# Kernel tuning notes

Hardware: AMD Instinct MI355X
Metric: run time of the kernel (lower is better)

The kernel has to match this reference:

```python
import jax, jax.numpy as jnp
import numpy as np

CODEBOOK_SIZE = 1024
LATENT_DIM = 64
BETA = 0.25

def setup_inputs() -> dict:
    key = jax.random.key(0)
    k1, k2 = jax.random.split(key)
    B, C, T = 32, LATENT_DIM, 4096
    x = jax.random.normal(k1, (B, C, T), dtype=jnp.float32)
    # codebook initialized uniform(-1/K, 1/K) as in the torch module
    emb = jax.random.uniform(k2, (CODEBOOK_SIZE, LATENT_DIM), dtype=jnp.float32,
                             minval=-1.0 / CODEBOOK_SIZE, maxval=1.0 / CODEBOOK_SIZE)
    return {"x": x, "emb": emb}

def reference(x, emb):
    B, C, T = x.shape  # C == LATENT_DIM
    xf = jnp.transpose(x, (0, 2, 1)).reshape(B * T, C)  # [BT, D]
    d = (jnp.sum(xf * xf, axis=-1, keepdims=True)
         + jnp.sum(emb * emb, axis=-1)[None, :]
         - 2.0 * jnp.matmul(xf, emb.T))  # [BT, K]
    idx = jnp.argmin(d, axis=-1)  # [BT] int
    q = emb[idx].reshape(B, T, C).transpose(0, 2, 1)  # [B, C, T]
    commitment_loss = BETA * jnp.mean((jax.lax.stop_gradient(q) - x) ** 2)
    codebook_loss = jnp.mean((q - jax.lax.stop_gradient(x)) ** 2)
    quant_out = x + jax.lax.stop_gradient(q - x)  # straight-through
    return quant_out, codebook_loss, commitment_loss, idx.reshape(B, T)
```

## Files before the change

### kernel.cpp

```cpp
#include <hip/hip_runtime.h>


typedef unsigned long long u64;
typedef unsigned short u16;
typedef __attribute__((ext_vector_type(8))) short bf8_t;
typedef __attribute__((ext_vector_type(4))) float f4_t;

#define KCB 1024
#define DD 64
#define BB 32
#define TT 4096
#define BT (BB * TT)
#define NELEM (BB * DD * TT)

#define RPB 128
#define NT 16
#define FB_MAX 48
#define BAND 4e-5f

#define WS_LOSS 0
#define WS_E2 64
#define WS_EH 2048
#define WS_EL 34816

static __device__ __forceinline__ u16 bf16rte(float f) {
    unsigned u = __float_as_uint(f);
    return (u16)((u + 0x7FFFu + ((u >> 16) & 1u)) >> 16);
}
static __device__ __forceinline__ unsigned flipf(float f) {
    unsigned u = __float_as_uint(f);
    return (u & 0x80000000u) ? ~u : (u | 0x80000000u);
}
static __device__ __forceinline__ int fragidx(int n, int d) {
    return 1024 * (n >> 4) + 512 * (d >> 5) + 128 * ((d >> 3) & 3)
         + 8 * (n & 15) + (d & 7);
}

__global__ void vq_prep(const float* __restrict__ emb, float* __restrict__ ws) {
#pragma clang fp contract(off)
    const int tid = threadIdx.x;
    const int kl = tid >> 6, d = tid & 63;
    const int k = blockIdx.x * 4 + kl;
    if (blockIdx.x == 0 && tid == 0) ws[WS_LOSS] = 0.0f;
    __shared__ float sq[4][64];
    __shared__ float rsh[4][8];
    float v = emb[(size_t)k * DD + d];
    u16 hb = bf16rte(v);
    float hv = __uint_as_float((unsigned)hb << 16);
    u16 lb = bf16rte(v - hv);
    u16* ehg = (u16*)(ws + WS_EH) + 4096 * (k >> 6);
    u16* elg = (u16*)(ws + WS_EL) + 4096 * (k >> 6);
    const int ia = fragidx(k & 63, d);
    ehg[ia] = hb; elg[ia] = lb;
    sq[kl][d] = v * v;
    __syncthreads();
    if (tid < 32) {
        const int g = tid >> 3, j = tid & 7;
        float r = sq[g][j];
#pragma unroll
        for (int i = 1; i < 8; ++i) r += sq[g][8 * i + j];
        rsh[g][j] = r;
    }
    __syncthreads();
    if (tid < 4) {
        const float* r = rsh[tid];
        ws[WS_E2 + blockIdx.x * 4 + tid] =
            ((r[0] + r[1]) + (r[2] + r[3])) + ((r[4] + r[5]) + (r[6] + r[7]));
    }
}

__launch_bounds__(256, 4)
__global__ void vq_main(const float* __restrict__ x, const float* __restrict__ emb,
                        float* __restrict__ out, float* __restrict__ ws) {
#pragma clang fp contract(off)
    const int tid = threadIdx.x;
    const int lane = tid & 63;
    const int w = __builtin_amdgcn_readfirstlane(tid >> 6);
    const int l15 = lane & 15, q = lane >> 4;

    const int row0 = blockIdx.x * RPB;
    const int b = row0 >> 12;
    const int t0 = row0 & (TT - 1);

    __shared__ __align__(16) char arena[32768];
    u16* xhT = (u16*)arena;
    u16* xlT = (u16*)(arena + 16384);
    float* efs = (float*)arena;
    float* xfb = (float*)(arena + 16640);

    __shared__ float e2l[KCB];
    __shared__ float Srow[RPB];
    __shared__ int kwin[RPB];
    __shared__ int fbrows[FB_MAX];
    __shared__ int fbcnt;
    __shared__ float bsum;

    if (tid == 0) { fbcnt = 0; bsum = 0.0f; }
#pragma unroll
    for (int i = tid; i < KCB; i += 256) e2l[i] = ws[WS_E2 + i];

    if (tid < RPB) {
        const int r = tid;
        const float* xr = x + (size_t)b * DD * TT + t0 + r;
        const int gb = 1024 * (r >> 4);
        float rr[8];
#pragma unroll
        for (int i = 0; i < 64; i += 8) {
#pragma unroll
            for (int j = 0; j < 8; ++j) {
                float v = xr[(size_t)(i + j) * TT];
                if (i == 0) rr[j] = v * v; else rr[j] += v * v;
                u16 hb = bf16rte(v);
                float hv = __uint_as_float((unsigned)hb << 16);
                u16 lb = bf16rte(v - hv);
                const int ia = gb + fragidx(r & 15, i + j);
                xhT[ia] = hb; xlT[ia] = lb;
            }
        }
        Srow[r] = ((rr[0] + rr[1]) + (rr[2] + rr[3])) + ((rr[4] + rr[5]) + (rr[6] + rr[7]));
    }
    __syncthreads();

    bf8_t ah[2][2], al[2][2];
#pragma unroll
    for (int g = 0; g < 2; ++g) {
        const int gg = 2 * w + g;
        ah[g][0] = *(const bf8_t*)&xhT[1024 * gg + 8 * lane];
        ah[g][1] = *(const bf8_t*)&xhT[1024 * gg + 512 + 8 * lane];
        al[g][0] = *(const bf8_t*)&xlT[1024 * gg + 8 * lane];
        al[g][1] = *(const bf8_t*)&xlT[1024 * gg + 512 + 8 * lane];
    }
    float Sv[8];
#pragma unroll
    for (int g = 0; g < 2; ++g)
#pragma unroll
        for (int rg = 0; rg < 4; ++rg)
            Sv[4 * g + rg] = Srow[32 * w + 16 * g + 4 * q + rg];

    float v1[8], v2[8], kf[8];
#pragma unroll
    for (int s = 0; s < 8; ++s) { v1[s] = 3.4e38f; v2[s] = 3.4e38f; kf[s] = 0.0f; }

    const u16* ehg = (const u16*)(ws + WS_EH);
    const u16* elg = (const u16*)(ws + WS_EL);

#pragma unroll 1
    for (int T = 0; T < NT; ++T) {
#pragma unroll
        for (int cg = 0; cg < 4; ++cg) {
            const int kb = 64 * T + 16 * cg;
            const u16* bhp = ehg + 4096 * T + 1024 * cg;
            const u16* blp = elg + 4096 * T + 1024 * cg;
            bf8_t bh0 = *(const bf8_t*)&bhp[8 * lane];
            bf8_t bh1 = *(const bf8_t*)&bhp[512 + 8 * lane];
            bf8_t bl0 = *(const bf8_t*)&blp[8 * lane];
            bf8_t bl1 = *(const bf8_t*)&blp[512 + 8 * lane];
            const float e2v = e2l[kb + l15];
            const float kcol = (float)(kb + l15);
#pragma unroll
            for (int g = 0; g < 2; ++g) {
                f4_t acc = (f4_t){0.f, 0.f, 0.f, 0.f};
                acc = __builtin_amdgcn_mfma_f32_16x16x32_bf16(ah[g][0], bh0, acc, 0, 0, 0);
                acc = __builtin_amdgcn_mfma_f32_16x16x32_bf16(ah[g][0], bl0, acc, 0, 0, 0);
                acc = __builtin_amdgcn_mfma_f32_16x16x32_bf16(al[g][0], bh0, acc, 0, 0, 0);
                acc = __builtin_amdgcn_mfma_f32_16x16x32_bf16(ah[g][1], bh1, acc, 0, 0, 0);
                acc = __builtin_amdgcn_mfma_f32_16x16x32_bf16(ah[g][1], bl1, acc, 0, 0, 0);
                acc = __builtin_amdgcn_mfma_f32_16x16x32_bf16(al[g][1], bh1, acc, 0, 0, 0);
#pragma unroll
                for (int rg = 0; rg < 4; ++rg) {
                    const int s = 4 * g + rg;
                    float ck = Sv[s] + e2v;
                    float u = __builtin_fmaf(-2.0f, acc[rg], ck);
                    bool lt = u < v1[s];
                    float sp = lt ? v1[s] : u;
                    v2[s] = fminf(v2[s], sp);
                    kf[s] = lt ? kcol : kf[s];
                    v1[s] = fminf(v1[s], u);
                }
            }
        }
    }

#pragma unroll
    for (int m = 1; m < 16; m <<= 1) {
#pragma unroll
        for (int s = 0; s < 8; ++s) {
            float ov1 = __shfl_xor(v1[s], m, 16);
            float okf = __shfl_xor(kf[s], m, 16);
            float ov2 = __shfl_xor(v2[s], m, 16);
            float nmx = fmaxf(v1[s], ov1);
            v2[s] = fminf(fminf(v2[s], ov2), nmx);
            bool lt = ov1 < v1[s];
            kf[s] = lt ? okf : kf[s];
            v1[s] = fminf(v1[s], ov1);
        }
    }
    if (l15 == 0) {
#pragma unroll
        for (int g = 0; g < 2; ++g)
#pragma unroll
            for (int rg = 0; rg < 4; ++rg) {
                const int s = 4 * g + rg;
                const int r = 32 * w + 16 * g + 4 * q + rg;
                kwin[r] = (int)kf[s];
                if (v2[s] <= v1[s] + BAND) {
                    int i = atomicAdd(&fbcnt, 1);
                    if (i < FB_MAX) fbrows[i] = r;
                }
            }
    }
    __syncthreads();

    const int cnt = min(fbcnt, FB_MAX);
    if (cnt > 0) {
        for (int i = tid; i < cnt * 64; i += 256) {
            int fi = i >> 6, l = i & 63;
            xfb[fi * 65 + l] = x[(size_t)b * DD * TT + (size_t)l * TT + t0 + fbrows[fi]];
        }
        u64 pmin[12];
#pragma unroll
        for (int sl = 0; sl < 12; ++sl) pmin[sl] = ~0ull;
#pragma unroll 1
        for (int T2 = 0; T2 < NT; ++T2) {
            __syncthreads();
            {
                const int n = tid >> 2, qd = (tid & 3) * 16;
                const float* sp = emb + (size_t)(T2 * 64 + n) * DD + qd;
                float* dp = efs + n * 65 + qd;
#pragma unroll
                for (int j = 0; j < 16; ++j) dp[j] = sp[j];
            }
            __syncthreads();
#pragma unroll
            for (int sl = 0; sl < 12; ++sl) {
                const int fi = w + 4 * sl;
                if (fi < cnt) {
                    float acc = 0.0f;
#pragma unroll
                    for (int i = 0; i < 64; ++i)
                        acc = __builtin_fmaf(efs[lane * 65 + i], xfb[fi * 65 + i], acc);
                    float ck = Srow[fbrows[fi]] + e2l[T2 * 64 + lane];
                    float u = __builtin_fmaf(-2.0f, acc, ck);
                    u64 pk = ((u64)flipf(u) << 10) | (unsigned)(T2 * 64 + lane);
                    pmin[sl] = pmin[sl] < pk ? pmin[sl] : pk;
                }
            }
        }
#pragma unroll
        for (int sl = 0; sl < 12; ++sl) {
            const int fi = w + 4 * sl;
            if (fi < cnt) {
                u64 pk = pmin[sl];
#pragma unroll
                for (int dl = 32; dl > 0; dl >>= 1) {
                    u64 o = __shfl_xor(pk, dl);
                    pk = o < pk ? o : pk;
                }
                if (lane == 0) kwin[fbrows[fi]] = (int)(pk & 1023u);
            }
        }
        __syncthreads();
    }

    if (tid < RPB) out[NELEM + 2 + row0 + tid] = (float)kwin[tid];

    const int r = tid & 127, c0 = (tid >> 7) * 32;
    const int kw = kwin[r];
    const float* eqr = emb + (size_t)kw * DD;
    float lsum = 0.0f;
#pragma unroll 8
    for (int i = 0; i < 32; ++i) {
        const int c = c0 + i;
        const size_t o = (size_t)b * DD * TT + (size_t)c * TT + t0 + r;
        float qv = eqr[c];
        float xv = x[o];
        out[o] = qv;
        float a = qv - xv;
        lsum = __builtin_fmaf(a, a, lsum);
    }
#pragma unroll
    for (int off = 32; off > 0; off >>= 1) lsum += __shfl_down(lsum, off);
    if (lane == 0) atomicAdd(&bsum, lsum);
    __syncthreads();
    if (tid == 0) atomicAdd(ws + WS_LOSS, bsum);
}

__global__ void vq_finalize(const float* __restrict__ ws, float* __restrict__ out) {
    if (threadIdx.x == 0 && blockIdx.x == 0) {
        float M = ws[WS_LOSS] / (float)NELEM;
        out[NELEM + 0] = M;
        out[NELEM + 1] = 0.25f * M;
    }
}

extern "C" void kernel_launch(void* const* d_in, const int* in_sizes, int n_in,
                              void* d_out, int out_size, void* d_ws, size_t ws_size,
                              hipStream_t stream) {
    const float* x = (const float*)d_in[0];
    const float* emb = (const float*)d_in[1];
    float* out = (float*)d_out;
    float* ws = (float*)d_ws;

    vq_prep<<<KCB / 4, 256, 0, stream>>>(emb, ws);
    vq_main<<<BT / RPB, 256, 0, stream>>>(x, emb, out, ws);
    vq_finalize<<<1, 64, 0, stream>>>(ws, out);
}
```

Baseline: 204.5 us.

## Halve rows per block, stage codebook tiles in LDS, shuffle fallback x

Rows per block drop from 128 to 64, with one 16-row MFMA group per wave, and the occupancy hint rises from 4 to 6 blocks per CU. Each 64-code tile of the bf16 hi/lo codebook fragments is now copied cooperatively into shared memory instead of every wave loading it from global memory. The near-tie fallback keeps x values in registers and broadcasts them with shuffles rather than staging them in LDS, which shrinks shared memory use. The costs are twice as many blocks, two extra barriers per tile, and half the MFMA work per codebook fragment load.

```diff
diff --git a/kernel.cpp b/kernel.cpp
--- a/kernel.cpp
+++ b/kernel.cpp
@@ -13,9 +13,10 @@
 #define BT (BB * TT)
 #define NELEM (BB * DD * TT)
 
-#define RPB 128
+#define RPB 64
 #define NT 16
-#define FB_MAX 48
+#define FB_MAX 24
+#define NSL 6
 #define BAND 4e-5f
 
 #define WS_LOSS 0
@@ -69,7 +70,7 @@
     }
 }
 
-__launch_bounds__(256, 4)
+__launch_bounds__(256, 6)
 __global__ void vq_main(const float* __restrict__ x, const float* __restrict__ emb,
                         float* __restrict__ out, float* __restrict__ ws) {
 #pragma clang fp contract(off)
@@ -82,13 +83,14 @@
     const int b = row0 >> 12;
     const int t0 = row0 & (TT - 1);
 
-    __shared__ __align__(16) char arena[32768];
+    __shared__ float e2l[KCB];
+    __shared__ __align__(16) char arena[16640];
     u16* xhT = (u16*)arena;
-    u16* xlT = (u16*)(arena + 16384);
+    u16* xlT = (u16*)(arena + 8192);
+    u16* Bh  = (u16*)arena;
+    u16* Bl  = (u16*)(arena + 8192);
     float* efs = (float*)arena;
-    float* xfb = (float*)(arena + 16640);
-
-    __shared__ float e2l[KCB];
+
     __shared__ float Srow[RPB];
     __shared__ int kwin[RPB];
     __shared__ int fbrows[FB_MAX];
@@ -121,70 +123,70 @@
     }
     __syncthreads();
 
-    bf8_t ah[2][2], al[2][2];
-#pragma unroll
-    for (int g = 0; g < 2; ++g) {
-        const int gg = 2 * w + g;
-        ah[g][0] = *(const bf8_t*)&xhT[1024 * gg + 8 * lane];
-        ah[g][1] = *(const bf8_t*)&xhT[1024 * gg + 512 + 8 * lane];
-        al[g][0] = *(const bf8_t*)&xlT[1024 * gg + 8 * lane];
-        al[g][1] = *(const bf8_t*)&xlT[1024 * gg + 512 + 8 * lane];
-    }
-    float Sv[8];
-#pragma unroll
-    for (int g = 0; g < 2; ++g)
-#pragma unroll
-        for (int rg = 0; rg < 4; ++rg)
-            Sv[4 * g + rg] = Srow[32 * w + 16 * g + 4 * q + rg];
-
-    float v1[8], v2[8], kf[8];
-#pragma unroll
-    for (int s = 0; s < 8; ++s) { v1[s] = 3.4e38f; v2[s] = 3.4e38f; kf[s] = 0.0f; }
+    bf8_t ah[2], al[2];
+    ah[0] = *(const bf8_t*)&xhT[1024 * w + 8 * lane];
+    ah[1] = *(const bf8_t*)&xhT[1024 * w + 512 + 8 * lane];
+    al[0] = *(const bf8_t*)&xlT[1024 * w + 8 * lane];
+    al[1] = *(const bf8_t*)&xlT[1024 * w + 512 + 8 * lane];
+    float Sv[4];
+#pragma unroll
+    for (int rg = 0; rg < 4; ++rg) Sv[rg] = Srow[16 * w + 4 * q + rg];
+    __syncthreads();
+
+    float v1[4], v2[4], kf[4];
+#pragma unroll
+    for (int s = 0; s < 4; ++s) { v1[s] = 3.4e38f; v2[s] = 3.4e38f; kf[s] = 0.0f; }
 
     const u16* ehg = (const u16*)(ws + WS_EH);
     const u16* elg = (const u16*)(ws + WS_EL);
 
 #pragma unroll 1
     for (int T = 0; T < NT; ++T) {
+        {
+            const f4_t* gh = (const f4_t*)(ehg + 4096 * T);
+            const f4_t* gl = (const f4_t*)(elg + 4096 * T);
+            f4_t* dh = (f4_t*)Bh;
+            f4_t* dl = (f4_t*)Bl;
+            dh[tid] = gh[tid];
+            dh[tid + 256] = gh[tid + 256];
+            dl[tid] = gl[tid];
+            dl[tid + 256] = gl[tid + 256];
+        }
+        __syncthreads();
 #pragma unroll
         for (int cg = 0; cg < 4; ++cg) {
             const int kb = 64 * T + 16 * cg;
-            const u16* bhp = ehg + 4096 * T + 1024 * cg;
-            const u16* blp = elg + 4096 * T + 1024 * cg;
-            bf8_t bh0 = *(const bf8_t*)&bhp[8 * lane];
-            bf8_t bh1 = *(const bf8_t*)&bhp[512 + 8 * lane];
-            bf8_t bl0 = *(const bf8_t*)&blp[8 * lane];
-            bf8_t bl1 = *(const bf8_t*)&blp[512 + 8 * lane];
+            bf8_t bh0 = *(const bf8_t*)&Bh[1024 * cg + 8 * lane];
+            bf8_t bh1 = *(const bf8_t*)&Bh[1024 * cg + 512 + 8 * lane];
+            bf8_t bl0 = *(const bf8_t*)&Bl[1024 * cg + 8 * lane];
+            bf8_t bl1 = *(const bf8_t*)&Bl[1024 * cg + 512 + 8 * lane];
             const float e2v = e2l[kb + l15];
             const float kcol = (float)(kb + l15);
-#pragma unroll
-            for (int g = 0; g < 2; ++g) {
-                f4_t acc = (f4_t){0.f, 0.f, 0.f, 0.f};
-                acc = __builtin_amdgcn_mfma_f32_16x16x32_bf16(ah[g][0], bh0, acc, 0, 0, 0);
-                acc = __builtin_amdgcn_mfma_f32_16x16x32_bf16(ah[g][0], bl0, acc, 0, 0, 0);
-                acc = __builtin_amdgcn_mfma_f32_16x16x32_bf16(al[g][0], bh0, acc, 0, 0, 0);
-                acc = __builtin_amdgcn_mfma_f32_16x16x32_bf16(ah[g][1], bh1, acc, 0, 0, 0);
-                acc = __builtin_amdgcn_mfma_f32_16x16x32_bf16(ah[g][1], bl1, acc, 0, 0, 0);
-                acc = __builtin_amdgcn_mfma_f32_16x16x32_bf16(al[g][1], bh1, acc, 0, 0, 0);
-#pragma unroll
-                for (int rg = 0; rg < 4; ++rg) {
-                    const int s = 4 * g + rg;
-                    float ck = Sv[s] + e2v;
-                    float u = __builtin_fmaf(-2.0f, acc[rg], ck);
-                    bool lt = u < v1[s];
-                    float sp = lt ? v1[s] : u;
-                    v2[s] = fminf(v2[s], sp);
-                    kf[s] = lt ? kcol : kf[s];
-                    v1[s] = fminf(v1[s], u);
-                }
-            }
-        }
+            f4_t acc = (f4_t){0.f, 0.f, 0.f, 0.f};
+            acc = __builtin_amdgcn_mfma_f32_16x16x32_bf16(ah[0], bh0, acc, 0, 0, 0);
+            acc = __builtin_amdgcn_mfma_f32_16x16x32_bf16(ah[0], bl0, acc, 0, 0, 0);
+            acc = __builtin_amdgcn_mfma_f32_16x16x32_bf16(al[0], bh0, acc, 0, 0, 0);
+            acc = __builtin_amdgcn_mfma_f32_16x16x32_bf16(ah[1], bh1, acc, 0, 0, 0);
+            acc = __builtin_amdgcn_mfma_f32_16x16x32_bf16(ah[1], bl1, acc, 0, 0, 0);
+            acc = __builtin_amdgcn_mfma_f32_16x16x32_bf16(al[1], bh1, acc, 0, 0, 0);
+#pragma unroll
+            for (int rg = 0; rg < 4; ++rg) {
+                float ck = Sv[rg] + e2v;
+                float u = __builtin_fmaf(-2.0f, acc[rg], ck);
+                bool lt = u < v1[rg];
+                float sp = lt ? v1[rg] : u;
+                v2[rg] = fminf(v2[rg], sp);
+                kf[rg] = lt ? kcol : kf[rg];
+                v1[rg] = fminf(v1[rg], u);
+            }
+        }
+        __syncthreads();
     }
 
 #pragma unroll
     for (int m = 1; m < 16; m <<= 1) {
 #pragma unroll
-        for (int s = 0; s < 8; ++s) {
+        for (int s = 0; s < 4; ++s) {
             float ov1 = __shfl_xor(v1[s], m, 16);
             float okf = __shfl_xor(kf[s], m, 16);
             float ov2 = __shfl_xor(v2[s], m, 16);
@@ -197,29 +199,31 @@
     }
     if (l15 == 0) {
 #pragma unroll
-        for (int g = 0; g < 2; ++g)
-#pragma unroll
-            for (int rg = 0; rg < 4; ++rg) {
-                const int s = 4 * g + rg;
-                const int r = 32 * w + 16 * g + 4 * q + rg;
-                kwin[r] = (int)kf[s];
-                if (v2[s] <= v1[s] + BAND) {
-                    int i = atomicAdd(&fbcnt, 1);
-                    if (i < FB_MAX) fbrows[i] = r;
-                }
-            }
+        for (int rg = 0; rg < 4; ++rg) {
+            const int r = 16 * w + 4 * q + rg;
+            kwin[r] = (int)kf[rg];
+            if (v2[rg] <= v1[rg] + BAND) {
+                int i = atomicAdd(&fbcnt, 1);
+                if (i < FB_MAX) fbrows[i] = r;
+            }
+        }
     }
     __syncthreads();
 
     const int cnt = min(fbcnt, FB_MAX);
     if (cnt > 0) {
-        for (int i = tid; i < cnt * 64; i += 256) {
-            int fi = i >> 6, l = i & 63;
-            xfb[fi * 65 + l] = x[(size_t)b * DD * TT + (size_t)l * TT + t0 + fbrows[fi]];
-        }
-        u64 pmin[12];
-#pragma unroll
-        for (int sl = 0; sl < 12; ++sl) pmin[sl] = ~0ull;
+        float xv[NSL], srw[NSL];
+        u64 pmin[NSL];
+#pragma unroll
+        for (int sl = 0; sl < NSL; ++sl) {
+            pmin[sl] = ~0ull;
+            const int fi = w + 4 * sl;
+            if (fi < cnt) {
+                const int fr = fbrows[fi];
+                xv[sl] = x[(size_t)b * DD * TT + (size_t)lane * TT + t0 + fr];
+                srw[sl] = Srow[fr];
+            }
+        }
 #pragma unroll 1
         for (int T2 = 0; T2 < NT; ++T2) {
             __syncthreads();
@@ -232,14 +236,14 @@
             }
             __syncthreads();
 #pragma unroll
-            for (int sl = 0; sl < 12; ++sl) {
+            for (int sl = 0; sl < NSL; ++sl) {
                 const int fi = w + 4 * sl;
                 if (fi < cnt) {
                     float acc = 0.0f;
 #pragma unroll
                     for (int i = 0; i < 64; ++i)
-                        acc = __builtin_fmaf(efs[lane * 65 + i], xfb[fi * 65 + i], acc);
-                    float ck = Srow[fbrows[fi]] + e2l[T2 * 64 + lane];
+                        acc = __builtin_fmaf(efs[lane * 65 + i], __shfl(xv[sl], i), acc);
+                    float ck = srw[sl] + e2l[T2 * 64 + lane];
                     float u = __builtin_fmaf(-2.0f, acc, ck);
                     u64 pk = ((u64)flipf(u) << 10) | (unsigned)(T2 * 64 + lane);
                     pmin[sl] = pmin[sl] < pk ? pmin[sl] : pk;
@@ -247,7 +251,7 @@
             }
         }
 #pragma unroll
-        for (int sl = 0; sl < 12; ++sl) {
+        for (int sl = 0; sl < NSL; ++sl) {
             const int fi = w + 4 * sl;
             if (fi < cnt) {
                 u64 pk = pmin[sl];
@@ -264,18 +268,18 @@
 
     if (tid < RPB) out[NELEM + 2 + row0 + tid] = (float)kwin[tid];
 
-    const int r = tid & 127, c0 = (tid >> 7) * 32;
+    const int r = tid & 63, c0 = (tid >> 6) * 16;
     const int kw = kwin[r];
     const float* eqr = emb + (size_t)kw * DD;
     float lsum = 0.0f;
 #pragma unroll 8
-    for (int i = 0; i < 32; ++i) {
+    for (int i = 0; i < 16; ++i) {
         const int c = c0 + i;
         const size_t o = (size_t)b * DD * TT + (size_t)c * TT + t0 + r;
         float qv = eqr[c];
-        float xv = x[o];
+        float xw = x[o];
         out[o] = qv;
-        float a = qv - xv;
+        float a = qv - xw;
         lsum = __builtin_fmaf(a, a, lsum);
     }
 #pragma unroll
```

Result: slower. 236.4 us (+15.6%).

## Drop shared-memory arena, build MFMA fragments from global loads, shuffle-based fallback

Applied to the files above, without the earlier changes.

Removes the 32KB shared arena. Each lane now loads its own MFMA A-fragment elements straight from global memory and splits them into hi/lo bf16 in registers, with no LDS staging. The fallback exact-distance path now works per flagged row, broadcasting x with lane shuffles and reading codebook rows directly from global instead of staging them in LDS with block syncs. Occupancy is raised from 4 to 6 blocks per CU. The cost is uncoalesced strided global loads for the fragments, more shuffles, and register pressure under the tighter launch bound.

```diff
diff --git a/kernel.cpp b/kernel.cpp
--- a/kernel.cpp
+++ b/kernel.cpp
@@ -16,6 +16,7 @@
 #define RPB 128
 #define NT 16
 #define FB_MAX 48
+#define NSL 12
 #define BAND 4e-5f
 
 #define WS_LOSS 0
@@ -69,7 +70,7 @@
     }
 }
 
-__launch_bounds__(256, 4)
+__launch_bounds__(256, 6)
 __global__ void vq_main(const float* __restrict__ x, const float* __restrict__ emb,
                         float* __restrict__ out, float* __restrict__ ws) {
 #pragma clang fp contract(off)
@@ -82,12 +83,6 @@
     const int b = row0 >> 12;
     const int t0 = row0 & (TT - 1);
 
-    __shared__ __align__(16) char arena[32768];
-    u16* xhT = (u16*)arena;
-    u16* xlT = (u16*)(arena + 16384);
-    float* efs = (float*)arena;
-    float* xfb = (float*)(arena + 16640);
-
     __shared__ float e2l[KCB];
     __shared__ float Srow[RPB];
     __shared__ int kwin[RPB];
@@ -99,37 +94,42 @@
 #pragma unroll
     for (int i = tid; i < KCB; i += 256) e2l[i] = ws[WS_E2 + i];
 
+    const float* xb = x + (size_t)b * DD * TT + t0;
+
     if (tid < RPB) {
         const int r = tid;
-        const float* xr = x + (size_t)b * DD * TT + t0 + r;
-        const int gb = 1024 * (r >> 4);
         float rr[8];
 #pragma unroll
         for (int i = 0; i < 64; i += 8) {
 #pragma unroll
             for (int j = 0; j < 8; ++j) {
-                float v = xr[(size_t)(i + j) * TT];
+                float v = xb[(size_t)(i + j) * TT + r];
                 if (i == 0) rr[j] = v * v; else rr[j] += v * v;
+            }
+        }
+        Srow[r] = ((rr[0] + rr[1]) + (rr[2] + rr[3])) + ((rr[4] + rr[5]) + (rr[6] + rr[7]));
+    }
+
+    bf8_t ah[2][2], al[2][2];
+#pragma unroll
+    for (int g = 0; g < 2; ++g) {
+        const int rbase = 16 * (2 * w + g) + l15;
+#pragma unroll
+        for (int h = 0; h < 2; ++h) {
+            const int dbase = 32 * h + 8 * q;
+#pragma unroll
+            for (int j = 0; j < 8; ++j) {
+                float v = xb[(size_t)(dbase + j) * TT + rbase];
                 u16 hb = bf16rte(v);
                 float hv = __uint_as_float((unsigned)hb << 16);
                 u16 lb = bf16rte(v - hv);
-                const int ia = gb + fragidx(r & 15, i + j);
-                xhT[ia] = hb; xlT[ia] = lb;
-            }
-        }
-        Srow[r] = ((rr[0] + rr[1]) + (rr[2] + rr[3])) + ((rr[4] + rr[5]) + (rr[6] + rr[7]));
-    }
-    __syncthreads();
-
-    bf8_t ah[2][2], al[2][2];
-#pragma unroll
-    for (int g = 0; g < 2; ++g) {
-        const int gg = 2 * w + g;
-        ah[g][0] = *(const bf8_t*)&xhT[1024 * gg + 8 * lane];
-        ah[g][1] = *(const bf8_t*)&xhT[1024 * gg + 512 + 8 * lane];
-        al[g][0] = *(const bf8_t*)&xlT[1024 * gg + 8 * lane];
-        al[g][1] = *(const bf8_t*)&xlT[1024 * gg + 512 + 8 * lane];
-    }
+                ah[g][h][j] = (short)hb;
+                al[g][h][j] = (short)lb;
+            }
+        }
+    }
+    __syncthreads();
+
     float Sv[8];
 #pragma unroll
     for (int g = 0; g < 2; ++g)
@@ -213,50 +213,32 @@
 
     const int cnt = min(fbcnt, FB_MAX);
     if (cnt > 0) {
-        for (int i = tid; i < cnt * 64; i += 256) {
-            int fi = i >> 6, l = i & 63;
-            xfb[fi * 65 + l] = x[(size_t)b * DD * TT + (size_t)l * TT + t0 + fbrows[fi]];
-        }
-        u64 pmin[12];
-#pragma unroll
-        for (int sl = 0; sl < 12; ++sl) pmin[sl] = ~0ull;
 #pragma unroll 1
-        for (int T2 = 0; T2 < NT; ++T2) {
-            __syncthreads();
-            {
-                const int n = tid >> 2, qd = (tid & 3) * 16;
-                const float* sp = emb + (size_t)(T2 * 64 + n) * DD + qd;
-                float* dp = efs + n * 65 + qd;
-#pragma unroll
-                for (int j = 0; j < 16; ++j) dp[j] = sp[j];
-            }
-            __syncthreads();
-#pragma unroll
-            for (int sl = 0; sl < 12; ++sl) {
-                const int fi = w + 4 * sl;
-                if (fi < cnt) {
+        for (int sl = 0; sl < NSL; ++sl) {
+            const int fi = w + 4 * sl;
+            if (fi < cnt) {
+                const int fr = fbrows[fi];
+                const float xv = x[(size_t)b * DD * TT + (size_t)lane * TT + t0 + fr];
+                const float srw = Srow[fr];
+                u64 pmin = ~0ull;
+#pragma unroll 1
+                for (int T2 = 0; T2 < NT; ++T2) {
+                    const float* er = emb + (size_t)(T2 * 64 + lane) * DD;
                     float acc = 0.0f;
 #pragma unroll
                     for (int i = 0; i < 64; ++i)
-                        acc = __builtin_fmaf(efs[lane * 65 + i], xfb[fi * 65 + i], acc);
-                    float ck = Srow[fbrows[fi]] + e2l[T2 * 64 + lane];
+                        acc = __builtin_fmaf(er[i], __shfl(xv, i), acc);
+                    float ck = srw + e2l[T2 * 64 + lane];
                     float u = __builtin_fmaf(-2.0f, acc, ck);
                     u64 pk = ((u64)flipf(u) << 10) | (unsigned)(T2 * 64 + lane);
-                    pmin[sl] = pmin[sl] < pk ? pmin[sl] : pk;
-                }
-            }
-        }
-#pragma unroll
-        for (int sl = 0; sl < 12; ++sl) {
-            const int fi = w + 4 * sl;
-            if (fi < cnt) {
-                u64 pk = pmin[sl];
+                    pmin = pmin < pk ? pmin : pk;
+                }
 #pragma unroll
                 for (int dl = 32; dl > 0; dl >>= 1) {
-                    u64 o = __shfl_xor(pk, dl);
-                    pk = o < pk ? o : pk;
-                }
-                if (lane == 0) kwin[fbrows[fi]] = (int)(pk & 1023u);
+                    u64 o = __shfl_xor(pmin, dl);
+                    pmin = o < pmin ? o : pmin;
+                }
+                if (lane == 0) kwin[fr] = (int)(pmin & 1023u);
             }
         }
         __syncthreads();
```

New measurement: 509.9 us. 2.49x slower.

## Stage codebook fragments through LDS with triple-buffered async global_load_lds pipeline

Applied to the files above, without the earlier changes.

Each codebook chunk (hi and lo bf16 fragments) used to be loaded by every wave straight from global memory. Now each wave issues one asynchronous global-to-LDS copy of its quarter of the chunk into a three-slot ring buffer, two chunks ahead. All waves then read the chunk from LDS. The intent is to share codebook loads across waves and hide global latency behind the MFMA work. The cost is a block barrier every iteration plus manual waitcnt handling. The code relies on an `arena` LDS buffer that is not defined in the visible hunks.

```diff
diff --git a/kernel.cpp b/kernel.cpp
--- a/kernel.cpp
+++ b/kernel.cpp
@@ -34,6 +34,11 @@
 static __device__ __forceinline__ int fragidx(int n, int d) {
     return 1024 * (n >> 4) + 512 * (d >> 5) + 128 * ((d >> 3) & 3)
          + 8 * (n & 15) + (d & 7);
+}
+static __device__ __forceinline__ void gload_lds16(const void* g, void* l) {
+    __builtin_amdgcn_global_load_lds(
+        (const __attribute__((address_space(1))) void*)g,
+        (__attribute__((address_space(3))) void*)l, 16, 0, 0);
 }
 
 __global__ void vq_prep(const float* __restrict__ emb, float* __restrict__ ws) {
@@ -144,41 +149,78 @@
     const u16* ehg = (const u16*)(ws + WS_EH);
     const u16* elg = (const u16*)(ws + WS_EL);
 
+    auto kstep = [&](float e2v, float kcol,
+                     bf8_t bh0, bf8_t bl0, bf8_t bh1, bf8_t bl1) {
+#pragma unroll
+        for (int g = 0; g < 2; ++g) {
+            f4_t acc = (f4_t){0.f, 0.f, 0.f, 0.f};
+            acc = __builtin_amdgcn_mfma_f32_16x16x32_bf16(ah[g][0], bh0, acc, 0, 0, 0);
+            acc = __builtin_amdgcn_mfma_f32_16x16x32_bf16(ah[g][0], bl0, acc, 0, 0, 0);
+            acc = __builtin_amdgcn_mfma_f32_16x16x32_bf16(al[g][0], bh0, acc, 0, 0, 0);
+            acc = __builtin_amdgcn_mfma_f32_16x16x32_bf16(ah[g][1], bh1, acc, 0, 0, 0);
+            acc = __builtin_amdgcn_mfma_f32_16x16x32_bf16(ah[g][1], bl1, acc, 0, 0, 0);
+            acc = __builtin_amdgcn_mfma_f32_16x16x32_bf16(al[g][1], bh1, acc, 0, 0, 0);
+#pragma unroll
+            for (int rg = 0; rg < 4; ++rg) {
+                const int s = 4 * g + rg;
+                float ck = Sv[s] + e2v;
+                float u = __builtin_fmaf(-2.0f, acc[rg], ck);
+                bool lt = u < v1[s];
+                float sp = lt ? v1[s] : u;
+                v2[s] = fminf(v2[s], sp);
+                kf[s] = lt ? kcol : kf[s];
+                v1[s] = fminf(v1[s], u);
+            }
+        }
+    };
+
+    const u16* psrc = (w < 2) ? ehg : elg;
+    const int poff = (w & 1) * 512;
+    char* const pdst0 = arena + 1024 * w;
+    auto issue = [&](int it2, int bufi) {
+        gload_lds16(psrc + 1024 * it2 + poff + 8 * lane, pdst0 + 4096 * bufi);
+    };
+
+    __syncthreads();
+    issue(0, 0);
+    issue(1, 1);
+    asm volatile("s_waitcnt vmcnt(1)" ::: "memory");
+    __builtin_amdgcn_s_barrier();
+#pragma unroll 3
+    for (int it = 0; it < 60; ++it) {
+        const int cur = it % 3;
+        const u16* bb = (const u16*)(arena + 4096 * cur);
+        bf8_t bh0 = *(const bf8_t*)&bb[8 * lane];
+        bf8_t bh1 = *(const bf8_t*)&bb[512 + 8 * lane];
+        bf8_t bl0 = *(const bf8_t*)&bb[1024 + 8 * lane];
+        bf8_t bl1 = *(const bf8_t*)&bb[1536 + 8 * lane];
+        const float e2v = e2l[16 * it + l15];
+        asm volatile("s_waitcnt lgkmcnt(0)" ::: "memory");
+        __builtin_amdgcn_sched_barrier(0);
+        issue(it + 2, (it + 2) % 3);
+        kstep(e2v, (float)(16 * it + l15), bh0, bl0, bh1, bl1);
+        asm volatile("s_waitcnt vmcnt(1)" ::: "memory");
+        __builtin_amdgcn_s_barrier();
+    }
 #pragma unroll 1
-    for (int T = 0; T < NT; ++T) {
-#pragma unroll
-        for (int cg = 0; cg < 4; ++cg) {
-            const int kb = 64 * T + 16 * cg;
-            const u16* bhp = ehg + 4096 * T + 1024 * cg;
-            const u16* blp = elg + 4096 * T + 1024 * cg;
-            bf8_t bh0 = *(const bf8_t*)&bhp[8 * lane];
-            bf8_t bh1 = *(const bf8_t*)&bhp[512 + 8 * lane];
-            bf8_t bl0 = *(const bf8_t*)&blp[8 * lane];
-            bf8_t bl1 = *(const bf8_t*)&blp[512 + 8 * lane];
-            const float e2v = e2l[kb + l15];
-            const float kcol = (float)(kb + l15);
-#pragma unroll
-            for (int g = 0; g < 2; ++g) {
-                f4_t acc = (f4_t){0.f, 0.f, 0.f, 0.f};
-                acc = __builtin_amdgcn_mfma_f32_16x16x32_bf16(ah[g][0], bh0, acc, 0, 0, 0);
-                acc = __builtin_amdgcn_mfma_f32_16x16x32_bf16(ah[g][0], bl0, acc, 0, 0, 0);
-                acc = __builtin_amdgcn_mfma_f32_16x16x32_bf16(al[g][0], bh0, acc, 0, 0, 0);
-                acc = __builtin_amdgcn_mfma_f32_16x16x32_bf16(ah[g][1], bh1, acc, 0, 0, 0);
-                acc = __builtin_amdgcn_mfma_f32_16x16x32_bf16(ah[g][1], bl1, acc, 0, 0, 0);
-                acc = __builtin_amdgcn_mfma_f32_16x16x32_bf16(al[g][1], bh1, acc, 0, 0, 0);
-#pragma unroll
-                for (int rg = 0; rg < 4; ++rg) {
-                    const int s = 4 * g + rg;
-                    float ck = Sv[s] + e2v;
-                    float u = __builtin_fmaf(-2.0f, acc[rg], ck);
-                    bool lt = u < v1[s];
-                    float sp = lt ? v1[s] : u;
-                    v2[s] = fminf(v2[s], sp);
-                    kf[s] = lt ? kcol : kf[s];
-                    v1[s] = fminf(v1[s], u);
-                }
-            }
-        }
+    for (int it = 60; it < 64; ++it) {
+        const int cur = it % 3;
+        const u16* bb = (const u16*)(arena + 4096 * cur);
+        bf8_t bh0 = *(const bf8_t*)&bb[8 * lane];
+        bf8_t bh1 = *(const bf8_t*)&bb[512 + 8 * lane];
+        bf8_t bl0 = *(const bf8_t*)&bb[1024 + 8 * lane];
+        bf8_t bl1 = *(const bf8_t*)&bb[1536 + 8 * lane];
+        const float e2v = e2l[16 * it + l15];
+        asm volatile("s_waitcnt lgkmcnt(0)" ::: "memory");
+        __builtin_amdgcn_sched_barrier(0);
+        if (it < 62) issue(it + 2, (it + 2) % 3);
+        kstep(e2v, (float)(16 * it + l15), bh0, bl0, bh1, bl1);
+        if (it < 62) {
+            asm volatile("s_waitcnt vmcnt(1)" ::: "memory");
+        } else {
+            asm volatile("s_waitcnt vmcnt(0)" ::: "memory");
+        }
+        __builtin_amdgcn_s_barrier();
     }
 
 #pragma unroll
```

After: 198.3 us. -3.0%, faster.
